# Optimization experiments

Hardware: AMD Instinct MI355X
Metric: run time of the kernel (lower is better)

Reference implementation:

```python
import jax, jax.numpy as jnp
import numpy as np

D_MODEL = 1024
NUM_HEADS = 16
THETA = 10000.0


def setup_inputs() -> dict:
    key = jax.random.key(0)
    ks = jax.random.split(key, 5)
    B, S, D = 4, 2048, D_MODEL
    std = float(np.sqrt(2.0 / (D + D)))
    x = jax.random.normal(ks[0], (B, S, D), dtype=jnp.float32)
    wq = jax.random.normal(ks[1], (D, D), dtype=jnp.float32) * std
    wk = jax.random.normal(ks[2], (D, D), dtype=jnp.float32) * std
    wv = jax.random.normal(ks[3], (D, D), dtype=jnp.float32) * std
    wo = jax.random.normal(ks[4], (D, D), dtype=jnp.float32) * std
    token_positions = jnp.broadcast_to(jnp.arange(S, dtype=jnp.int32), (B, S))
    return {"x": x, "token_positions": token_positions,
            "wq": wq, "wk": wk, "wv": wv, "wo": wo}


def _rope(t, token_positions, d_k):
    # t: [B, H, S, d_k]; token_positions: [B, S]
    freqs = 1.0 / (THETA ** (jnp.arange(0, d_k, 2, dtype=jnp.float32) / d_k))  # [d_k/2]
    angles = token_positions.astype(jnp.float32)[..., None] * freqs            # [B, S, d_k/2]
    angles = jnp.repeat(angles, 2, axis=-1)                                    # [B, S, d_k]
    cos = jnp.cos(angles)[:, None, :, :]  # broadcast over heads
    sin = jnp.sin(angles)[:, None, :, :]
    t1, t2 = t[..., 0::2], t[..., 1::2]
    t_rot = jnp.stack([-t2, t1], axis=-1).reshape(t.shape)  # interleave (-x2, x1)
    return t * cos + t_rot * sin


def reference(x, token_positions, wq, wk, wv, wo):
    B, S, D = x.shape
    H = NUM_HEADS
    d_k = D // H
    def proj(w):
        return (x @ w.T).reshape(B, S, H, d_k).transpose(0, 2, 1, 3)  # [B,H,S,dk]
    q = _rope(proj(wq), token_positions, d_k)
    k = _rope(proj(wk), token_positions, d_k)
    v = proj(wv)
    scale = 1.0 / jnp.sqrt(jnp.float32(d_k))
    scores = jnp.einsum('bhqd,bhkd->bhqk', q, k) * scale  # [B,H,S,S]
    causal = jnp.tril(jnp.ones((S, S), dtype=bool))
    scores = jnp.where(causal, scores, -jnp.inf)
    attn = jax.nn.softmax(scores, axis=-1)
    out = jnp.einsum('bhqk,bhkd->bhqd', attn, v)          # [B,H,S,dk]
    out = out.transpose(0, 2, 1, 3).reshape(B, S, D)
    return out @ wo.T
```

## Files before the change

kernel.cpp:

```cpp
#include <hip/hip_runtime.h>
#include <hip/hip_bf16.h>
#include <cstdint>
#include <cstddef>

#define B_ 4
#define S_ 2048
#define D_ 1024
#define H_ 16
#define DK_ 64
#define NTOK (B_*S_)

typedef __bf16 bf16;
typedef __bf16 bf16x8 __attribute__((ext_vector_type(8)));
typedef short s16x4 __attribute__((ext_vector_type(4)));
typedef float f32x4 __attribute__((ext_vector_type(4)));

#define AS1 __attribute__((address_space(1)))
#define AS3 __attribute__((address_space(3)))

static __device__ __forceinline__ short f2bf_s(float f) {
    return __builtin_bit_cast(short, (__bf16)f);
}

static __device__ __forceinline__ f32x4 mfma16(s16x4 a, s16x4 b, f32x4 c) {
#if __has_builtin(__builtin_amdgcn_mfma_f32_16x16x16bf16_1k)
    return __builtin_amdgcn_mfma_f32_16x16x16bf16_1k(a, b, c, 0, 0, 0);
#else
    asm volatile("v_mfma_f32_16x16x16_bf16 %0, %1, %2, %0\n\ts_nop 7\n\ts_nop 7"
                 : "+v"(c) : "v"(a), "v"(b));
    return c;
#endif
}

__global__ void cvt_all(const float* __restrict__ x, const float* __restrict__ wq,
                        const float* __restrict__ wk, const float* __restrict__ wv,
                        const float* __restrict__ wo, bf16* __restrict__ dst) {
    const int NX8 = NTOK * D_ / 8;
    const int W8 = D_ * D_ / 8;
    int i = blockIdx.x * blockDim.x + threadIdx.x;
    if (i >= NX8 + 4 * W8) return;
    const float* src; int j;
    if (i < NX8) { src = x; j = i; }
    else {
        int k = i - NX8;
        int w = k >> 17;
        j = k & (W8 - 1);
        src = w == 0 ? wq : (w == 1 ? wk : (w == 2 ? wv : wo));
    }
    const float4* s4 = reinterpret_cast<const float4*>(src) + (size_t)j * 2;
    float4 a = s4[0], b = s4[1];
    bf16x8 o;
    o[0] = (bf16)a.x; o[1] = (bf16)a.y; o[2] = (bf16)a.z; o[3] = (bf16)a.w;
    o[4] = (bf16)b.x; o[5] = (bf16)b.y; o[6] = (bf16)b.z; o[7] = (bf16)b.w;
    reinterpret_cast<bf16x8*>(dst)[i] = o;
}

__global__ void rope_table(const int* __restrict__ pos, float2* __restrict__ tab) {
    int i = blockIdx.x * blockDim.x + threadIdx.x;
    if (i >= NTOK * 32) return;
    int n = i >> 5, p = i & 31;
    float pf = (float)pos[n];
    float freq = powf(10000.0f, -(float)p * (1.0f / 32.0f));
    float ang = pf * freq;
    float s, c;
    sincosf(ang, &s, &c);
    tab[i] = make_float2(c, s);
}

template<int MODE>
__global__ __launch_bounds__(512, 2)
void gemm256(const bf16* __restrict__ A, const bf16* __restrict__ Bw,
             void* __restrict__ OutP, const float2* __restrict__ tab) {
    const float SCL2E = 0.125f * 1.44269504088896340736f;
    constexpr int NKT = 16;
    __shared__ alignas(16) bf16 lds[2][(256 + 128) * 64];
    const int tid = threadIdx.x;
    const int lane = tid & 63;
    const int wid = tid >> 6;
    const int wm = wid >> 2;
    const int wn = wid & 3;
    const int lr = lane & 15, lg = lane >> 4;
    const int m0 = blockIdx.x * 256;
    const int n0g = blockIdx.y * 128;

    f32x4 acc[8][2] = {};

    auto stage = [&](int kt, int bufi) {
        bf16* dst = &lds[bufi][0];
#pragma unroll
        for (int j = 0; j < 4; ++j) {
            int flat = j * 512 + tid;
            int r = flat >> 3, c = flat & 7;
            const bf16* src = A + (size_t)(m0 + r) * 1024 + kt * 64 + ((c ^ (r & 7)) << 3);
            __builtin_amdgcn_global_load_lds((const AS1 uint32_t*)src,
                                             (AS3 uint32_t*)(dst + (size_t)flat * 8), 16, 0, 0);
        }
#pragma unroll
        for (int j = 0; j < 2; ++j) {
            int f2 = j * 512 + tid;
            int r = f2 >> 3, c = f2 & 7;
            const bf16* src = Bw + (size_t)(n0g + r) * 1024 + kt * 64 + ((c ^ (r & 7)) << 3);
            __builtin_amdgcn_global_load_lds((const AS1 uint32_t*)src,
                                             (AS3 uint32_t*)(dst + 256 * 64 + (size_t)f2 * 8), 16, 0, 0);
        }
    };

    stage(0, 0);

    for (int kt = 0; kt < NKT; ++kt) {
        const bf16* bufA = &lds[kt & 1][0];
        const bf16* bufB = bufA + 256 * 64;

        asm volatile("" ::: "memory");
        __builtin_amdgcn_s_barrier();
        asm volatile("" ::: "memory");
        if (kt + 1 < NKT) {
            stage(kt + 1, (kt + 1) & 1);
            asm volatile("s_waitcnt vmcnt(6)" ::: "memory");
        } else {
            asm volatile("s_waitcnt vmcnt(0)" ::: "memory");
        }
        __builtin_amdgcn_s_barrier();
        asm volatile("" ::: "memory");

        const int sx = lr & 7;
        bf16x8 af[4][2], bfr[2][2];
#pragma unroll
        for (int mf = 0; mf < 4; ++mf)
#pragma unroll
            for (int kh = 0; kh < 2; ++kh)
                af[mf][kh] = *reinterpret_cast<const bf16x8*>(
                    &bufA[(wm * 128 + mf * 16 + lr) * 64 + (((kh * 4 + lg) ^ sx) << 3)]);
#pragma unroll
        for (int kh = 0; kh < 2; ++kh)
            bfr[0][kh] = *reinterpret_cast<const bf16x8*>(
                &bufB[(wn * 32 + lr) * 64 + (((kh * 4 + lg) ^ sx) << 3)]);
#pragma unroll
        for (int mf = 0; mf < 4; ++mf)
#pragma unroll
            for (int kh = 0; kh < 2; ++kh)
                acc[mf][0] = __builtin_amdgcn_mfma_f32_16x16x32_bf16(af[mf][kh], bfr[0][kh], acc[mf][0], 0, 0, 0);
#pragma unroll
        for (int kh = 0; kh < 2; ++kh)
            bfr[1][kh] = *reinterpret_cast<const bf16x8*>(
                &bufB[(wn * 32 + 16 + lr) * 64 + (((kh * 4 + lg) ^ sx) << 3)]);
#pragma unroll
        for (int mf = 0; mf < 4; ++mf)
#pragma unroll
            for (int kh = 0; kh < 2; ++kh)
                acc[mf][1] = __builtin_amdgcn_mfma_f32_16x16x32_bf16(af[mf][kh], bfr[1][kh], acc[mf][1], 0, 0, 0);
#pragma unroll
        for (int mf = 0; mf < 4; ++mf)
#pragma unroll
            for (int kh = 0; kh < 2; ++kh)
                af[mf][kh] = *reinterpret_cast<const bf16x8*>(
                    &bufA[(wm * 128 + 64 + mf * 16 + lr) * 64 + (((kh * 4 + lg) ^ sx) << 3)]);
#pragma unroll
        for (int mf = 0; mf < 4; ++mf)
#pragma unroll
            for (int kh = 0; kh < 2; ++kh)
                acc[4 + mf][0] = __builtin_amdgcn_mfma_f32_16x16x32_bf16(af[mf][kh], bfr[0][kh], acc[4 + mf][0], 0, 0, 0);
#pragma unroll
        for (int mf = 0; mf < 4; ++mf)
#pragma unroll
            for (int kh = 0; kh < 2; ++kh)
                acc[4 + mf][1] = __builtin_amdgcn_mfma_f32_16x16x32_bf16(af[mf][kh], bfr[1][kh], acc[4 + mf][1], 0, 0, 0);
    }

#pragma unroll
    for (int mf = 0; mf < 8; ++mf) {
#pragma unroll
        for (int nf = 0; nf < 2; ++nf) {
#pragma unroll
            for (int r = 0; r < 4; ++r) {
                int row = m0 + wm * 128 + mf * 16 + lg * 4 + r;
                int colg = n0g + wn * 32 + nf * 16 + lr;
                float v = acc[mf][nf][r];
                if (MODE == 2) {
                    ((float*)OutP)[(size_t)row * 1024 + colg] = v;
                } else {
                    int which = colg >> 10;
                    int col = colg & 1023;
                    bf16* O = (bf16*)OutP + (size_t)which * NTOK * D_;
                    if (which < 2) {
                        float partner = __shfl_xor(v, 1, 64);
                        float2 cs = tab[(size_t)row * 32 + ((col >> 1) & 31)];
                        float o = (col & 1) ? fmaf(v, cs.x, partner * cs.y)
                                            : fmaf(v, cs.x, -partner * cs.y);
                        if (which == 0) o *= SCL2E;
                        O[(size_t)row * D_ + col] = (bf16)o;
                    } else {
                        O[(size_t)row * D_ + col] = (bf16)v;
                    }
                }
            }
        }
    }
}

__global__ __launch_bounds__(256, 2)
void flash_attn5(const bf16* __restrict__ Q, const bf16* __restrict__ Kr,
                 const bf16* __restrict__ V, bf16* __restrict__ O) {
    __shared__ bf16 Ks[2][64 * 64];
    __shared__ bf16 Vt[2][64 * 64];
    const int tid = threadIdx.x, lane = tid & 63, w = tid >> 6;
    const int lr = lane & 15, lg = lane >> 4;
    const int qtA = blockIdx.x;
    const int qtB = 15 - qtA;
    const int q0[2] = { qtA * 128, qtB * 128 };
    const int ntS[2] = { 2 * qtA + 2, 2 * qtB + 2 };
    const int NT = ntS[1];
    const int bh = blockIdx.y;
    const int b = bh >> 4, h = bh & 15;
    const size_t base = ((size_t)b * S_) * D_ + (size_t)h * DK_;

    bf16x8 aq[2][2][2];
#pragma unroll
    for (int si = 0; si < 2; ++si)
#pragma unroll
        for (int qs = 0; qs < 2; ++qs) {
            int qrow = q0[si] + w * 32 + qs * 16 + lr;
            const bf16* qp = Q + base + (size_t)qrow * D_ + lg * 8;
            aq[si][qs][0] = *reinterpret_cast<const bf16x8*>(qp);
            aq[si][qs][1] = *reinterpret_cast<const bf16x8*>(qp + 32);
        }

    f32x4 acc[2][2][4] = {};
    float m_run[2][2] = {{-1e30f, -1e30f}, {-1e30f, -1e30f}};
    float l_run[2][2] = {{0.f, 0.f}, {0.f, 0.f}};

    const int sjj = tid >> 3;
    const int se0 = (tid & 7) * 8;
    const int vx = tid & 7;
    bf16x8 kreg[2], vreg[2];
#pragma unroll
    for (int i = 0; i < 2; ++i) {
        int row = sjj + i * 32;
        kreg[i] = *reinterpret_cast<const bf16x8*>(&Kr[base + (size_t)row * D_ + se0]);
        vreg[i] = *reinterpret_cast<const bf16x8*>(&V [base + (size_t)row * D_ + se0]);
    }

    for (int t = 0; t < NT; ++t) {
        const int j0 = t * 64;
        bf16* KsB = Ks[t & 1];
        bf16* VtB = Vt[t & 1];
#pragma unroll
        for (int i = 0; i < 2; ++i) {
            int jj = sjj + i * 32;
            *reinterpret_cast<bf16x8*>(&KsB[jj * 64 + (se0 ^ ((jj & 7) << 3))]) = kreg[i];
#pragma unroll
            for (int q = 0; q < 8; ++q) {
                int dd = se0 + q;
                int vswz = ((q ^ vx) & 7) << 3;
                VtB[dd * 64 + (jj ^ vswz)] = vreg[i][q];
            }
        }
        if (t + 1 < NT) {
#pragma unroll
            for (int i = 0; i < 2; ++i) {
                int row = (t + 1) * 64 + sjj + i * 32;
                kreg[i] = *reinterpret_cast<const bf16x8*>(&Kr[base + (size_t)row * D_ + se0]);
                vreg[i] = *reinterpret_cast<const bf16x8*>(&V [base + (size_t)row * D_ + se0]);
            }
        }
        __syncthreads();

#pragma unroll
        for (int si = 0; si < 2; ++si) {
            if (t >= ntS[si]) continue;
            const int qmaxw = q0[si] + w * 32 + 31;
            if (j0 > qmaxw) continue;

            f32x4 sc[2][4];
            __builtin_amdgcn_s_setprio(1);
#pragma unroll
            for (int nt = 0; nt < 4; ++nt) {
                int krow = nt * 16 + lr;
                int swz = (krow & 7) << 3;
                bf16x8 a0 = *reinterpret_cast<const bf16x8*>(&KsB[krow * 64 + ((lg * 8) ^ swz)]);
                bf16x8 a1 = *reinterpret_cast<const bf16x8*>(&KsB[krow * 64 + ((32 + lg * 8) ^ swz)]);
#pragma unroll
                for (int qs = 0; qs < 2; ++qs) {
                    f32x4 tv = {};
                    tv = __builtin_amdgcn_mfma_f32_16x16x32_bf16(a0, aq[si][qs][0], tv, 0, 0, 0);
                    tv = __builtin_amdgcn_mfma_f32_16x16x32_bf16(a1, aq[si][qs][1], tv, 0, 0, 0);
                    sc[qs][nt] = tv;
                }
            }
            __builtin_amdgcn_s_setprio(0);

            s16x4 ap[2][4];
#pragma unroll
            for (int qs = 0; qs < 2; ++qs) {
                const int qrow = q0[si] + w * 32 + qs * 16 + lr;
                if (j0 + 63 > q0[si] + w * 32 + qs * 16) {
#pragma unroll
                    for (int nt = 0; nt < 4; ++nt)
#pragma unroll
                        for (int r = 0; r < 4; ++r) {
                            int kv = j0 + nt * 16 + lg * 4 + r;
                            if (kv > qrow) sc[qs][nt][r] = -1e30f;
                        }
                }
                float tmax = sc[qs][0][0];
#pragma unroll
                for (int nt = 0; nt < 4; ++nt)
#pragma unroll
                    for (int r = 0; r < 4; ++r) tmax = fmaxf(tmax, sc[qs][nt][r]);
                tmax = fmaxf(tmax, __shfl_xor(tmax, 16, 64));
                tmax = fmaxf(tmax, __shfl_xor(tmax, 32, 64));
                float mold = m_run[si][qs];
                if (!__all(tmax - mold <= 8.0f)) {
                    float mnew = fmaxf(mold, tmax);
                    float corr = exp2f(mold - mnew);
                    m_run[si][qs] = mnew;
                    l_run[si][qs] *= corr;
#pragma unroll
                    for (int r = 0; r < 4; ++r) {
                        float cr = __shfl(corr, (lane & 48) | (lg * 4 + r), 64);
#pragma unroll
                        for (int dt = 0; dt < 4; ++dt) acc[si][qs][dt][r] *= cr;
                    }
                }
                float mnow = m_run[si][qs];
                float rs = 0.f;
#pragma unroll
                for (int nt = 0; nt < 4; ++nt)
#pragma unroll
                    for (int r = 0; r < 4; ++r) {
                        float p = exp2f(sc[qs][nt][r] - mnow);
                        rs += p;
                        ap[qs][nt][r] = f2bf_s(p);
                    }
                rs += __shfl_xor(rs, 16, 64);
                rs += __shfl_xor(rs, 32, 64);
                l_run[si][qs] += rs;
            }

            __builtin_amdgcn_s_setprio(1);
#pragma unroll
            for (int dt = 0; dt < 4; ++dt) {
                int vrow = dt * 16 + lr;
                int vswz = (((vrow & 7) ^ (vrow >> 3)) & 7) << 3;
                s16x4 bv[4];
#pragma unroll
                for (int nt = 0; nt < 4; ++nt)
                    bv[nt] = *reinterpret_cast<const s16x4*>(&VtB[vrow * 64 + ((nt * 16 + lg * 4) ^ vswz)]);
#pragma unroll
                for (int qs = 0; qs < 2; ++qs)
#pragma unroll
                    for (int nt = 0; nt < 4; ++nt)
                        acc[si][qs][dt] = mfma16(ap[qs][nt], bv[nt], acc[si][qs][dt]);
            }
            __builtin_amdgcn_s_setprio(0);
        }
    }

#pragma unroll
    for (int si = 0; si < 2; ++si)
#pragma unroll
        for (int qs = 0; qs < 2; ++qs) {
            float inv = __builtin_amdgcn_rcpf(l_run[si][qs]);
#pragma unroll
            for (int r = 0; r < 4; ++r) {
                float invr = __shfl(inv, (lane & 48) | (lg * 4 + r), 64);
                int row = q0[si] + w * 32 + qs * 16 + lg * 4 + r;
#pragma unroll
                for (int dt = 0; dt < 4; ++dt)
                    O[base + (size_t)row * D_ + dt * 16 + lr] = (bf16)(acc[si][qs][dt][r] * invr);
            }
        }
}

extern "C" void kernel_launch(void* const* d_in, const int* in_sizes, int n_in,
                              void* d_out, int out_size, void* d_ws, size_t ws_size,
                              hipStream_t stream) {
    const float* x  = (const float*)d_in[0];
    const int*   tp = (const int*)d_in[1];
    const float* wq = (const float*)d_in[2];
    const float* wk = (const float*)d_in[3];
    const float* wv = (const float*)d_in[4];
    const float* wo = (const float*)d_in[5];

    bf16* ws = (bf16*)d_ws;
    bf16* Xbf = ws;
    bf16* Wqb = Xbf + (size_t)NTOK * D_;
    bf16* Wkb = Wqb + (size_t)D_ * D_;
    bf16* Wvb = Wkb + (size_t)D_ * D_;
    bf16* Wob = Wvb + (size_t)D_ * D_;
    bf16* Qr  = Wob + (size_t)D_ * D_;
    bf16* Kb  = Qr + (size_t)NTOK * D_;
    bf16* Vb  = Kb + (size_t)NTOK * D_;
    bf16* AO  = Vb + (size_t)NTOK * D_;
    float2* tab = (float2*)(AO + (size_t)NTOK * D_);
    (void)ws_size; (void)in_sizes; (void)n_in; (void)out_size;
    (void)Wkb; (void)Wvb;

    {
        int ntot8 = (NTOK * D_ + 4 * D_ * D_) / 8;
        cvt_all<<<(ntot8 + 255) / 256, 256, 0, stream>>>(x, wq, wk, wv, wo, Xbf);
    }
    rope_table<<<(NTOK * 32 + 255) / 256, 256, 0, stream>>>(tp, tab);

    gemm256<1><<<dim3(NTOK / 256, 24), 512, 0, stream>>>(Xbf, Wqb, Qr, tab);

    flash_attn5<<<dim3(8, B_ * H_), 256, 0, stream>>>(Qr, Kb, Vb, AO);

    gemm256<2><<<dim3(NTOK / 256, D_ / 128), 512, 0, stream>>>(AO, Wob, d_out, nullptr);
}
```

Baseline: 208.8 us.

## Split paired causal q-tiles into one q-tile per block with higher occupancy

Replaces the flash-attention kernel that paired a short and long causal q-tile per block (8 blocks per head) with one q-tile per block (16 blocks per head), launched longest-first. The per-block register state halves, so launch bounds rise from 2 to 4 blocks per SIMD group, raising occupancy. The cost is that each K/V tile is now loaded separately for each q-tile rather than shared between two, and load balance now depends on the hardware's block scheduling instead of explicit pairing.

Measured after the change: 385.3 us. 84.5% more time.

```diff
diff --git a/kernel.cpp b/kernel.cpp
--- a/kernel.cpp
+++ b/kernel.cpp
@@ -198,36 +198,32 @@
     }
 }
 
-__global__ __launch_bounds__(256, 2)
-void flash_attn5(const bf16* __restrict__ Q, const bf16* __restrict__ Kr,
+__global__ __launch_bounds__(256, 4)
+void flash_attn6(const bf16* __restrict__ Q, const bf16* __restrict__ Kr,
                  const bf16* __restrict__ V, bf16* __restrict__ O) {
     __shared__ bf16 Ks[2][64 * 64];
     __shared__ bf16 Vt[2][64 * 64];
     const int tid = threadIdx.x, lane = tid & 63, w = tid >> 6;
     const int lr = lane & 15, lg = lane >> 4;
-    const int qtA = blockIdx.x;
-    const int qtB = 15 - qtA;
-    const int q0[2] = { qtA * 128, qtB * 128 };
-    const int ntS[2] = { 2 * qtA + 2, 2 * qtB + 2 };
-    const int NT = ntS[1];
+    const int qt = 15 - (int)blockIdx.x;
+    const int q0 = qt * 128;
+    const int NT = 2 * qt + 2;
     const int bh = blockIdx.y;
     const int b = bh >> 4, h = bh & 15;
     const size_t base = ((size_t)b * S_) * D_ + (size_t)h * DK_;
 
-    bf16x8 aq[2][2][2];
-#pragma unroll
-    for (int si = 0; si < 2; ++si)
-#pragma unroll
-        for (int qs = 0; qs < 2; ++qs) {
-            int qrow = q0[si] + w * 32 + qs * 16 + lr;
-            const bf16* qp = Q + base + (size_t)qrow * D_ + lg * 8;
-            aq[si][qs][0] = *reinterpret_cast<const bf16x8*>(qp);
-            aq[si][qs][1] = *reinterpret_cast<const bf16x8*>(qp + 32);
-        }
-
-    f32x4 acc[2][2][4] = {};
-    float m_run[2][2] = {{-1e30f, -1e30f}, {-1e30f, -1e30f}};
-    float l_run[2][2] = {{0.f, 0.f}, {0.f, 0.f}};
+    bf16x8 aq[2][2];
+#pragma unroll
+    for (int qs = 0; qs < 2; ++qs) {
+        int qrow = q0 + w * 32 + qs * 16 + lr;
+        const bf16* qp = Q + base + (size_t)qrow * D_ + lg * 8;
+        aq[qs][0] = *reinterpret_cast<const bf16x8*>(qp);
+        aq[qs][1] = *reinterpret_cast<const bf16x8*>(qp + 32);
+    }
+
+    f32x4 acc[2][4] = {};
+    float m_run[2] = {-1e30f, -1e30f};
+    float l_run[2] = {0.f, 0.f};
 
     const int sjj = tid >> 3;
     const int se0 = (tid & 7) * 8;
@@ -240,6 +236,8 @@
         vreg[i] = *reinterpret_cast<const bf16x8*>(&V [base + (size_t)row * D_ + se0]);
     }
 
+    const int qmaxw = q0 + w * 32 + 31;
+
     for (int t = 0; t < NT; ++t) {
         const int j0 = t * 64;
         bf16* KsB = Ks[t & 1];
@@ -265,12 +263,7 @@
         }
         __syncthreads();
 
-#pragma unroll
-        for (int si = 0; si < 2; ++si) {
-            if (t >= ntS[si]) continue;
-            const int qmaxw = q0[si] + w * 32 + 31;
-            if (j0 > qmaxw) continue;
-
+        if (j0 <= qmaxw) {
             f32x4 sc[2][4];
             __builtin_amdgcn_s_setprio(1);
 #pragma unroll
@@ -282,8 +275,8 @@
 #pragma unroll
                 for (int qs = 0; qs < 2; ++qs) {
                     f32x4 tv = {};
-                    tv = __builtin_amdgcn_mfma_f32_16x16x32_bf16(a0, aq[si][qs][0], tv, 0, 0, 0);
-                    tv = __builtin_amdgcn_mfma_f32_16x16x32_bf16(a1, aq[si][qs][1], tv, 0, 0, 0);
+                    tv = __builtin_amdgcn_mfma_f32_16x16x32_bf16(a0, aq[qs][0], tv, 0, 0, 0);
+                    tv = __builtin_amdgcn_mfma_f32_16x16x32_bf16(a1, aq[qs][1], tv, 0, 0, 0);
                     sc[qs][nt] = tv;
                 }
             }
@@ -292,8 +285,8 @@
             s16x4 ap[2][4];
 #pragma unroll
             for (int qs = 0; qs < 2; ++qs) {
-                const int qrow = q0[si] + w * 32 + qs * 16 + lr;
-                if (j0 + 63 > q0[si] + w * 32 + qs * 16) {
+                const int qrow = q0 + w * 32 + qs * 16 + lr;
+                if (j0 + 63 > q0 + w * 32 + qs * 16) {
 #pragma unroll
                     for (int nt = 0; nt < 4; ++nt)
 #pragma unroll
@@ -309,20 +302,20 @@
                     for (int r = 0; r < 4; ++r) tmax = fmaxf(tmax, sc[qs][nt][r]);
                 tmax = fmaxf(tmax, __shfl_xor(tmax, 16, 64));
                 tmax = fmaxf(tmax, __shfl_xor(tmax, 32, 64));
-                float mold = m_run[si][qs];
+                float mold = m_run[qs];
                 if (!__all(tmax - mold <= 8.0f)) {
                     float mnew = fmaxf(mold, tmax);
                     float corr = exp2f(mold - mnew);
-                    m_run[si][qs] = mnew;
-                    l_run[si][qs] *= corr;
+                    m_run[qs] = mnew;
+                    l_run[qs] *= corr;
 #pragma unroll
                     for (int r = 0; r < 4; ++r) {
                         float cr = __shfl(corr, (lane & 48) | (lg * 4 + r), 64);
 #pragma unroll
-                        for (int dt = 0; dt < 4; ++dt) acc[si][qs][dt][r] *= cr;
+                        for (int dt = 0; dt < 4; ++dt) acc[qs][dt][r] *= cr;
                     }
                 }
-                float mnow = m_run[si][qs];
+                float mnow = m_run[qs];
                 float rs = 0.f;
 #pragma unroll
                 for (int nt = 0; nt < 4; ++nt)
@@ -334,7 +327,7 @@
                     }
                 rs += __shfl_xor(rs, 16, 64);
                 rs += __shfl_xor(rs, 32, 64);
-                l_run[si][qs] += rs;
+                l_run[qs] += rs;
             }
 
             __builtin_amdgcn_s_setprio(1);
@@ -350,26 +343,24 @@
                 for (int qs = 0; qs < 2; ++qs)
 #pragma unroll
                     for (int nt = 0; nt < 4; ++nt)
-                        acc[si][qs][dt] = mfma16(ap[qs][nt], bv[nt], acc[si][qs][dt]);
+                        acc[qs][dt] = mfma16(ap[qs][nt], bv[nt], acc[qs][dt]);
             }
             __builtin_amdgcn_s_setprio(0);
         }
     }
 
 #pragma unroll
-    for (int si = 0; si < 2; ++si)
-#pragma unroll
-        for (int qs = 0; qs < 2; ++qs) {
-            float inv = __builtin_amdgcn_rcpf(l_run[si][qs]);
-#pragma unroll
-            for (int r = 0; r < 4; ++r) {
-                float invr = __shfl(inv, (lane & 48) | (lg * 4 + r), 64);
-                int row = q0[si] + w * 32 + qs * 16 + lg * 4 + r;
-#pragma unroll
-                for (int dt = 0; dt < 4; ++dt)
-                    O[base + (size_t)row * D_ + dt * 16 + lr] = (bf16)(acc[si][qs][dt][r] * invr);
-            }
-        }
+    for (int qs = 0; qs < 2; ++qs) {
+        float inv = __builtin_amdgcn_rcpf(l_run[qs]);
+#pragma unroll
+        for (int r = 0; r < 4; ++r) {
+            float invr = __shfl(inv, (lane & 48) | (lg * 4 + r), 64);
+            int row = q0 + w * 32 + qs * 16 + lg * 4 + r;
+#pragma unroll
+            for (int dt = 0; dt < 4; ++dt)
+                O[base + (size_t)row * D_ + dt * 16 + lr] = (bf16)(acc[qs][dt][r] * invr);
+        }
+    }
 }
 
 extern "C" void kernel_launch(void* const* d_in, const int* in_sizes, int n_in,
@@ -404,7 +395,7 @@
 
     gemm256<1><<<dim3(NTOK / 256, 24), 512, 0, stream>>>(Xbf, Wqb, Qr, tab);
 
-    flash_attn5<<<dim3(8, B_ * H_), 256, 0, stream>>>(Qr, Kb, Vb, AO);
+    flash_attn6<<<dim3(16, B_ * H_), 256, 0, stream>>>(Qr, Kb, Vb, AO);
 
     gemm256<2><<<dim3(NTOK / 256, D_ / 128), 512, 0, stream>>>(AO, Wob, d_out, nullptr);
 }
```

## Switch projection GEMMs to 128x128 tiles with 4 waves and 64x64 warp tiles

Applied to the files above, without the earlier changes.

Replaces the 256x128 block tile (8 waves, 128x32 per wave) with a 128x128 block tile (4 waves, 64x64 per wave) for the QKV and output projection GEMMs. Each wave now loads all B fragments up front and runs a single 4x4 MFMA block, wrapped in s_setprio to favour matrix issue. The goal is better register-level reuse per wave and twice as many blocks to fill the CUs. The cost is less A reuse per block and more global/LDS traffic for B.

Measured after the change: 206.3 us. No clear change (-1.2%).

```diff
diff --git a/kernel.cpp b/kernel.cpp
--- a/kernel.cpp
+++ b/kernel.cpp
@@ -68,40 +68,40 @@
 }
 
 template<int MODE>
-__global__ __launch_bounds__(512, 2)
-void gemm256(const bf16* __restrict__ A, const bf16* __restrict__ Bw,
+__global__ __launch_bounds__(256, 2)
+void gemm128(const bf16* __restrict__ A, const bf16* __restrict__ Bw,
              void* __restrict__ OutP, const float2* __restrict__ tab) {
     const float SCL2E = 0.125f * 1.44269504088896340736f;
     constexpr int NKT = 16;
-    __shared__ alignas(16) bf16 lds[2][(256 + 128) * 64];
+    __shared__ alignas(16) bf16 lds[2][(128 + 128) * 64];
     const int tid = threadIdx.x;
     const int lane = tid & 63;
     const int wid = tid >> 6;
-    const int wm = wid >> 2;
-    const int wn = wid & 3;
+    const int wm = wid >> 1;
+    const int wn = wid & 1;
     const int lr = lane & 15, lg = lane >> 4;
-    const int m0 = blockIdx.x * 256;
+    const int m0 = blockIdx.x * 128;
     const int n0g = blockIdx.y * 128;
 
-    f32x4 acc[8][2] = {};
+    f32x4 acc[4][4] = {};
 
     auto stage = [&](int kt, int bufi) {
         bf16* dst = &lds[bufi][0];
 #pragma unroll
         for (int j = 0; j < 4; ++j) {
-            int flat = j * 512 + tid;
+            int flat = j * 256 + tid;
             int r = flat >> 3, c = flat & 7;
             const bf16* src = A + (size_t)(m0 + r) * 1024 + kt * 64 + ((c ^ (r & 7)) << 3);
             __builtin_amdgcn_global_load_lds((const AS1 uint32_t*)src,
                                              (AS3 uint32_t*)(dst + (size_t)flat * 8), 16, 0, 0);
         }
 #pragma unroll
-        for (int j = 0; j < 2; ++j) {
-            int f2 = j * 512 + tid;
-            int r = f2 >> 3, c = f2 & 7;
+        for (int j = 0; j < 4; ++j) {
+            int flat = j * 256 + tid;
+            int r = flat >> 3, c = flat & 7;
             const bf16* src = Bw + (size_t)(n0g + r) * 1024 + kt * 64 + ((c ^ (r & 7)) << 3);
             __builtin_amdgcn_global_load_lds((const AS1 uint32_t*)src,
-                                             (AS3 uint32_t*)(dst + 256 * 64 + (size_t)f2 * 8), 16, 0, 0);
+                                             (AS3 uint32_t*)(dst + 128 * 64 + (size_t)flat * 8), 16, 0, 0);
         }
     };
 
@@ -109,14 +109,14 @@
 
     for (int kt = 0; kt < NKT; ++kt) {
         const bf16* bufA = &lds[kt & 1][0];
-        const bf16* bufB = bufA + 256 * 64;
+        const bf16* bufB = bufA + 128 * 64;
 
         asm volatile("" ::: "memory");
         __builtin_amdgcn_s_barrier();
         asm volatile("" ::: "memory");
         if (kt + 1 < NKT) {
             stage(kt + 1, (kt + 1) & 1);
-            asm volatile("s_waitcnt vmcnt(6)" ::: "memory");
+            asm volatile("s_waitcnt vmcnt(8)" ::: "memory");
         } else {
             asm volatile("s_waitcnt vmcnt(0)" ::: "memory");
         }
@@ -124,57 +124,38 @@
         asm volatile("" ::: "memory");
 
         const int sx = lr & 7;
-        bf16x8 af[4][2], bfr[2][2];
+        bf16x8 af[4][2], bfr[4][2];
 #pragma unroll
         for (int mf = 0; mf < 4; ++mf)
 #pragma unroll
             for (int kh = 0; kh < 2; ++kh)
                 af[mf][kh] = *reinterpret_cast<const bf16x8*>(
-                    &bufA[(wm * 128 + mf * 16 + lr) * 64 + (((kh * 4 + lg) ^ sx) << 3)]);
-#pragma unroll
-        for (int kh = 0; kh < 2; ++kh)
-            bfr[0][kh] = *reinterpret_cast<const bf16x8*>(
-                &bufB[(wn * 32 + lr) * 64 + (((kh * 4 + lg) ^ sx) << 3)]);
+                    &bufA[(wm * 64 + mf * 16 + lr) * 64 + (((kh * 4 + lg) ^ sx) << 3)]);
+#pragma unroll
+        for (int nf = 0; nf < 4; ++nf)
+#pragma unroll
+            for (int kh = 0; kh < 2; ++kh)
+                bfr[nf][kh] = *reinterpret_cast<const bf16x8*>(
+                    &bufB[(wn * 64 + nf * 16 + lr) * 64 + (((kh * 4 + lg) ^ sx) << 3)]);
+        __builtin_amdgcn_s_setprio(1);
 #pragma unroll
         for (int mf = 0; mf < 4; ++mf)
 #pragma unroll
-            for (int kh = 0; kh < 2; ++kh)
-                acc[mf][0] = __builtin_amdgcn_mfma_f32_16x16x32_bf16(af[mf][kh], bfr[0][kh], acc[mf][0], 0, 0, 0);
-#pragma unroll
-        for (int kh = 0; kh < 2; ++kh)
-            bfr[1][kh] = *reinterpret_cast<const bf16x8*>(
-                &bufB[(wn * 32 + 16 + lr) * 64 + (((kh * 4 + lg) ^ sx) << 3)]);
-#pragma unroll
-        for (int mf = 0; mf < 4; ++mf)
-#pragma unroll
-            for (int kh = 0; kh < 2; ++kh)
-                acc[mf][1] = __builtin_amdgcn_mfma_f32_16x16x32_bf16(af[mf][kh], bfr[1][kh], acc[mf][1], 0, 0, 0);
-#pragma unroll
-        for (int mf = 0; mf < 4; ++mf)
-#pragma unroll
-            for (int kh = 0; kh < 2; ++kh)
-                af[mf][kh] = *reinterpret_cast<const bf16x8*>(
-                    &bufA[(wm * 128 + 64 + mf * 16 + lr) * 64 + (((kh * 4 + lg) ^ sx) << 3)]);
-#pragma unroll
-        for (int mf = 0; mf < 4; ++mf)
-#pragma unroll
-            for (int kh = 0; kh < 2; ++kh)
-                acc[4 + mf][0] = __builtin_amdgcn_mfma_f32_16x16x32_bf16(af[mf][kh], bfr[0][kh], acc[4 + mf][0], 0, 0, 0);
-#pragma unroll
-        for (int mf = 0; mf < 4; ++mf)
-#pragma unroll
-            for (int kh = 0; kh < 2; ++kh)
-                acc[4 + mf][1] = __builtin_amdgcn_mfma_f32_16x16x32_bf16(af[mf][kh], bfr[1][kh], acc[4 + mf][1], 0, 0, 0);
-    }
-
-#pragma unroll
-    for (int mf = 0; mf < 8; ++mf) {
-#pragma unroll
-        for (int nf = 0; nf < 2; ++nf) {
+            for (int nf = 0; nf < 4; ++nf)
+#pragma unroll
+                for (int kh = 0; kh < 2; ++kh)
+                    acc[mf][nf] = __builtin_amdgcn_mfma_f32_16x16x32_bf16(af[mf][kh], bfr[nf][kh], acc[mf][nf], 0, 0, 0);
+        __builtin_amdgcn_s_setprio(0);
+    }
+
+#pragma unroll
+    for (int mf = 0; mf < 4; ++mf) {
+#pragma unroll
+        for (int nf = 0; nf < 4; ++nf) {
 #pragma unroll
             for (int r = 0; r < 4; ++r) {
-                int row = m0 + wm * 128 + mf * 16 + lg * 4 + r;
-                int colg = n0g + wn * 32 + nf * 16 + lr;
+                int row = m0 + wm * 64 + mf * 16 + lg * 4 + r;
+                int colg = n0g + wn * 64 + nf * 16 + lr;
                 float v = acc[mf][nf][r];
                 if (MODE == 2) {
                     ((float*)OutP)[(size_t)row * 1024 + colg] = v;
@@ -402,9 +383,9 @@
     }
     rope_table<<<(NTOK * 32 + 255) / 256, 256, 0, stream>>>(tp, tab);
 
-    gemm256<1><<<dim3(NTOK / 256, 24), 512, 0, stream>>>(Xbf, Wqb, Qr, tab);
+    gemm128<1><<<dim3(NTOK / 128, 24), 256, 0, stream>>>(Xbf, Wqb, Qr, tab);
 
     flash_attn5<<<dim3(8, B_ * H_), 256, 0, stream>>>(Qr, Kb, Vb, AO);
 
-    gemm256<2><<<dim3(NTOK / 256, D_ / 128), 512, 0, stream>>>(AO, Wob, d_out, nullptr);
-}
+    gemm128<2><<<dim3(NTOK / 128, D_ / 128), 256, 0, stream>>>(AO, Wob, d_out, nullptr);
+}
```
